# Kernel tuning notes

Measured on AMD Instinct MI355X. Metric: run time of the kernel, lower is better.

Reference implementation:

```python
import jax, jax.numpy as jnp
import numpy as np
import math

B, S, IN_DIM = 4, 2048, 512
D, H, L, FF = 256, 4, 4, 2048
HD = D // H
EPS = 1e-5


def _pos_encoding(S, D, dtype=jnp.float32):
    pos = jnp.arange(S, dtype=jnp.float32)[:, None]
    div = jnp.exp(jnp.arange(0, D, 2, dtype=jnp.float32) * (-math.log(10000.0) / D))
    pe = jnp.zeros((S, D), dtype=jnp.float32)
    pe = pe.at[:, 0::2].set(jnp.sin(pos * div))
    pe = pe.at[:, 1::2].set(jnp.cos(pos * div))
    return pe.astype(dtype)


def _layernorm(x, w, b):
    mu = jnp.mean(x, axis=-1, keepdims=True)
    var = jnp.var(x, axis=-1, keepdims=True)
    return (x - mu) * jax.lax.rsqrt(var + EPS) * w + b


def setup_inputs() -> dict:
    key = jax.random.key(0)
    ks = jax.random.split(key, 12)
    sc = 0.02
    inp = {
        "x": jax.random.normal(ks[0], (B, S, IN_DIM), dtype=jnp.float32),
        "W_in": jax.random.normal(ks[1], (D, IN_DIM), dtype=jnp.float32) * sc,
        "b_in": jnp.zeros((D,), dtype=jnp.float32),
        "qkv_w": jax.random.normal(ks[2], (L, 3 * D, D), dtype=jnp.float32) * sc,
        "qkv_b": jnp.zeros((L, 3 * D), dtype=jnp.float32),
        "out_w": jax.random.normal(ks[3], (L, D, D), dtype=jnp.float32) * sc,
        "out_b": jnp.zeros((L, D), dtype=jnp.float32),
        "ln1_w": jnp.ones((L, D), dtype=jnp.float32),
        "ln1_b": jnp.zeros((L, D), dtype=jnp.float32),
        "ff1_w": jax.random.normal(ks[4], (L, FF, D), dtype=jnp.float32) * sc,
        "ff1_b": jnp.zeros((L, FF), dtype=jnp.float32),
        "ff2_w": jax.random.normal(ks[5], (L, D, FF), dtype=jnp.float32) * sc,
        "ff2_b": jnp.zeros((L, D), dtype=jnp.float32),
        "ln2_w": jnp.ones((L, D), dtype=jnp.float32),
        "ln2_b": jnp.zeros((L, D), dtype=jnp.float32),
        "W_fc": jax.random.normal(ks[6], (IN_DIM, D), dtype=jnp.float32) * sc,
        "b_fc": jnp.zeros((IN_DIM,), dtype=jnp.float32),
    }
    return inp


def reference(x, W_in, b_in, qkv_w, qkv_b, out_w, out_b, ln1_w, ln1_b,
              ff1_w, ff1_b, ff2_w, ff2_b, ln2_w, ln2_b, W_fc, b_fc):
    # input projection + positional encoding (dropout=0 / eval)
    h = jnp.einsum('bsi,di->bsd', x, W_in) + b_in
    h = h + _pos_encoding(S, D, h.dtype)[None]

    scale = 1.0 / math.sqrt(HD)
    for l in range(L):
        # --- self-attention (unfused: explicit QK^T + softmax + V) ---
        qkv = jnp.einsum('bsd,ed->bse', h, qkv_w[l]) + qkv_b[l]  # [B,S,3D]
        q, k, v = jnp.split(qkv, 3, axis=-1)
        q = q.reshape(B, S, H, HD).transpose(0, 2, 1, 3)  # [B,H,S,HD]
        k = k.reshape(B, S, H, HD).transpose(0, 2, 1, 3)
        v = v.reshape(B, S, H, HD).transpose(0, 2, 1, 3)
        scores = jnp.einsum('bhqd,bhkd->bhqk', q, k) * scale  # [B,H,S,S]
        attn = jax.nn.softmax(scores, axis=-1)
        ctx = jnp.einsum('bhqk,bhkd->bhqd', attn, v)
        ctx = ctx.transpose(0, 2, 1, 3).reshape(B, S, D)
        sa = jnp.einsum('bsd,ed->bse', ctx, out_w[l]) + out_b[l]
        h = _layernorm(h + sa, ln1_w[l], ln1_b[l])  # post-norm
        # --- feed-forward (relu) ---
        ff = jax.nn.relu(jnp.einsum('bsd,fd->bsf', h, ff1_w[l]) + ff1_b[l])
        ff = jnp.einsum('bsf,df->bsd', ff, ff2_w[l]) + ff2_b[l]
        h = _layernorm(h + ff, ln2_w[l], ln2_b[l])

    # final projection from last time step
    return jnp.einsum('bd,od->bo', h[:, -1, :], W_fc) + b_fc  # [B, IN_DIM]
```

## Files before the change

kernel.cpp:

```cpp
#include <hip/hip_runtime.h>
#include <math.h>

#define S_LEN 2048
#define DMODEL 256
#define NHEAD 4
#define HDIM 64
#define NLAYER 4
#define FFDIM 2048
#define INDIM 512
#define BATCH 4
#define NTOK (BATCH * S_LEN)
#define EPSV 1e-5f
#define KSPLIT 4

typedef __attribute__((ext_vector_type(8))) short frag8;
typedef __attribute__((ext_vector_type(4))) float f32x4v;
typedef unsigned short u16;
typedef unsigned int u32;

__device__ __forceinline__ float pe_val(int s, int d) {
    const float c = 0.035977892f;
    float dv = expf(-(float)(d & ~1) * c);
    float arg = (float)s * dv;
    return (d & 1) ? cosf(arg) : sinf(arg);
}

__device__ __forceinline__ u16 f2bf(float f) {
    union { float f; unsigned u; } v; v.f = f;
    unsigned r = v.u + 0x7fffu + ((v.u >> 16) & 1u);
    return (u16)(r >> 16);
}
__device__ __forceinline__ float bf2f(u16 h) {
    union { u32 u; float f; } v; v.u = (u32)h << 16; return v.f;
}
__device__ __forceinline__ u32 pk2bf(float lo, float hi) {
    union { float f; u32 u; } a, b; a.f = lo; b.f = hi;
    return __builtin_amdgcn_perm(b.u, a.u, 0x07060302u);
}
__device__ __forceinline__ void load_lds16(const u16* g, u16* l) {
    __builtin_amdgcn_global_load_lds(
        (const __attribute__((address_space(1))) unsigned int*)g,
        (__attribute__((address_space(3))) unsigned int*)l, 16, 0, 0);
}

__global__ __launch_bounds__(256) void cvt_all(
    const float* __restrict__ x, const float* __restrict__ W_in,
    const float* __restrict__ qkv_w, const float* __restrict__ out_w,
    const float* __restrict__ ff1_w, const float* __restrict__ ff2_w,
    u16* __restrict__ xb, u16* __restrict__ W_in_b,
    u16* __restrict__ qkv_w_b, u16* __restrict__ out_w_b,
    u16* __restrict__ ff1_w_b, u16* __restrict__ ff2_w_b)
{
    const int i = blockIdx.x * 256 + threadIdx.x;
    const float* src; u16* dst; int base;
    if (i < 1048576)      { src = x;     dst = xb;      base = 0; }
    else if (i < 1081344) { src = W_in;  dst = W_in_b;  base = 1048576; }
    else if (i < 1277952) { src = qkv_w; dst = qkv_w_b; base = 1081344; }
    else if (i < 1343488) { src = out_w; dst = out_w_b; base = 1277952; }
    else if (i < 1867776) { src = ff1_w; dst = ff1_w_b; base = 1343488; }
    else                  { src = ff2_w; dst = ff2_w_b; base = 1867776; }
    const int e = (i - base) * 4;
    const float4 v = *(const float4*)(src + e);
    ushort4 o;
    o.x = f2bf(v.x); o.y = f2bf(v.y); o.z = f2bf(v.z); o.w = f2bf(v.w);
    *(ushort4*)(dst + e) = o;
}

template <int MODE>
__global__ __launch_bounds__(256) void gemm_mfma(
    const u16* __restrict__ A, const u16* __restrict__ W,
    const float* __restrict__ bias, u16* __restrict__ Cb,
    u16* __restrict__ vt, int M, int N, int K)
{
    __shared__ __align__(16) u16 As[128 * 32];
    __shared__ __align__(16) u16 Bs[128 * 32];
    const int t = threadIdx.x;
    const int w = t >> 6, lane = t & 63;
    const int col = lane & 15, quad = lane >> 4;
    const int qx = (quad ^ ((col >> 1) & 3)) * 8;
    const int m0 = blockIdx.x * 128, n0 = blockIdx.y * 128;
    const int wm = (w >> 1) * 64, wn = (w & 1) * 64;

    const int r0 = lane >> 2;
    const int kc = ((lane & 3) ^ ((lane >> 3) & 3)) * 8;
    const u16* pA0 = A + (size_t)(m0 + (w * 2 + 0) * 16 + r0) * K + kc;
    const u16* pA1 = A + (size_t)(m0 + (w * 2 + 1) * 16 + r0) * K + kc;
    const u16* pB0 = W + (size_t)(n0 + (w * 2 + 0) * 16 + r0) * K + kc;
    const u16* pB1 = W + (size_t)(n0 + (w * 2 + 1) * 16 + r0) * K + kc;
    u16* lA0 = As + (w * 2 + 0) * 512;
    u16* lA1 = As + (w * 2 + 1) * 512;
    u16* lB0 = Bs + (w * 2 + 0) * 512;
    u16* lB1 = Bs + (w * 2 + 1) * 512;

    f32x4v acc[4][4];
#pragma unroll
    for (int i = 0; i < 4; ++i)
#pragma unroll
        for (int j = 0; j < 4; ++j) acc[i][j] = (f32x4v){0.f, 0.f, 0.f, 0.f};

    for (int kb = 0; kb < K; kb += 32) {
        __syncthreads();
        load_lds16(pA0 + kb, lA0);
        load_lds16(pA1 + kb, lA1);
        load_lds16(pB0 + kb, lB0);
        load_lds16(pB1 + kb, lB1);
        __syncthreads();

        frag8 a[4], b[4];
#pragma unroll
        for (int i = 0; i < 4; ++i)
            a[i] = *(const frag8*)&As[(wm + i * 16 + col) * 32 + qx];
#pragma unroll
        for (int j = 0; j < 4; ++j)
            b[j] = *(const frag8*)&Bs[(wn + j * 16 + col) * 32 + qx];
#pragma unroll
        for (int i = 0; i < 4; ++i)
#pragma unroll
            for (int j = 0; j < 4; ++j)
                acc[i][j] = __builtin_amdgcn_mfma_f32_16x16x32_bf16(
                    a[i], b[j], acc[i][j], 0, 0, 0);
    }

#pragma unroll
    for (int j = 0; j < 4; ++j) {
        const int cn = n0 + wn + j * 16 + col;
        const float bv = bias[cn];
#pragma unroll
        for (int i = 0; i < 4; ++i) {
            const int cmb = m0 + wm + i * 16 + quad * 4;
            float vv[4];
#pragma unroll
            for (int r = 0; r < 4; ++r) {
                float v = acc[i][j][r] + bv;
                if (MODE == 2) v = fmaxf(v, 0.f);
                vv[r] = v;
                Cb[(size_t)(cmb + r) * N + cn] = f2bf(v);
            }
            if (MODE == 4 && cn >= 512) {
                const int dg = cn - 512;
                const int bh = (cmb >> 11) * 4 + (dg >> 6);
                uint2 pk;
                pk.x = ((u32)f2bf(vv[1]) << 16) | f2bf(vv[0]);
                pk.y = ((u32)f2bf(vv[3]) << 16) | f2bf(vv[2]);
                *(uint2*)&vt[((size_t)bh * 64 + (dg & 63)) * S_LEN + (cmb & 2047)] = pk;
            }
        }
    }
}

template <int MODE>
__global__ __launch_bounds__(256) void gemm64k(
    const u16* __restrict__ A, const u16* __restrict__ W,
    const float* __restrict__ bias, u16* __restrict__ Cb,
    int M, int N, int K)
{
    __shared__ __align__(16) u16 As[64 * 64];
    __shared__ __align__(16) u16 Bs[64 * 64];
    const int t = threadIdx.x;
    const int w = t >> 6, lane = t & 63;
    const int col = lane & 15, quad = lane >> 4;
    const int px0 = ((quad ^ (col & 7))) * 8;
    const int px1 = px0 ^ 32;
    const int m0 = blockIdx.x * 64, n0 = blockIdx.y * 64;
    const int wm = (w >> 1) * 32, wn = (w & 1) * 32;

    const int sr = lane >> 3;
    const int lc = ((lane & 7) ^ sr) * 8;
    const u16* pA0 = A + (size_t)(m0 + w * 16 + sr) * K + lc;
    const u16* pA1 = A + (size_t)(m0 + w * 16 + 8 + sr) * K + lc;
    const u16* pB0 = W + (size_t)(n0 + w * 16 + sr) * K + lc;
    const u16* pB1 = W + (size_t)(n0 + w * 16 + 8 + sr) * K + lc;
    u16* lA0 = As + (w * 16) * 64;
    u16* lA1 = As + (w * 16 + 8) * 64;
    u16* lB0 = Bs + (w * 16) * 64;
    u16* lB1 = Bs + (w * 16 + 8) * 64;

    f32x4v acc[2][2];
#pragma unroll
    for (int i = 0; i < 2; ++i)
#pragma unroll
        for (int j = 0; j < 2; ++j) acc[i][j] = (f32x4v){0.f, 0.f, 0.f, 0.f};

    for (int kb = 0; kb < K; kb += 64) {
        __syncthreads();
        load_lds16(pA0 + kb, lA0);
        load_lds16(pA1 + kb, lA1);
        load_lds16(pB0 + kb, lB0);
        load_lds16(pB1 + kb, lB1);
        __syncthreads();

#pragma unroll
        for (int kh = 0; kh < 2; ++kh) {
            const int px = kh ? px1 : px0;
            frag8 a[2], b[2];
#pragma unroll
            for (int i = 0; i < 2; ++i)
                a[i] = *(const frag8*)&As[(wm + i * 16 + col) * 64 + px];
#pragma unroll
            for (int j = 0; j < 2; ++j)
                b[j] = *(const frag8*)&Bs[(wn + j * 16 + col) * 64 + px];
#pragma unroll
            for (int i = 0; i < 2; ++i)
#pragma unroll
                for (int j = 0; j < 2; ++j)
                    acc[i][j] = __builtin_amdgcn_mfma_f32_16x16x32_bf16(
                        a[i], b[j], acc[i][j], 0, 0, 0);
        }
    }

#pragma unroll
    for (int j = 0; j < 2; ++j) {
        const int cn = n0 + wn + j * 16 + col;
        const float bv = bias[cn];
#pragma unroll
        for (int i = 0; i < 2; ++i) {
#pragma unroll
            for (int r = 0; r < 4; ++r) {
                const int cm = m0 + wm + i * 16 + quad * 4 + r;
                float v = acc[i][j][r] + bv;
                if (MODE == 1) v += pe_val(cm & (S_LEN - 1), cn);
                Cb[(size_t)cm * N + cn] = f2bf(v);
            }
        }
    }
}

__global__ __launch_bounds__(256) void attn_part(const u16* __restrict__ qkv,
                                                 const u16* __restrict__ vt,
                                                 float* __restrict__ Opart,
                                                 float* __restrict__ lpart)
{
    __shared__ __align__(16) u16 Ks0[64 * 32], Ks1[64 * 32];
    __shared__ __align__(16) u16 Vt0[64 * 32], Vt1[64 * 32];
    __shared__ __align__(16) u16 Ps[4][2][2][512];

    const int t = threadIdx.x;
    const int w = t >> 6, lane = t & 63;
    const int col = lane & 15, quad = lane >> 4;
    const int sq = (col >> 1) & 3;
    const int qx = (quad ^ sq) * 8;
    const int bh = blockIdx.x, b = bh >> 2, hh = bh & 3;
    const int qt = blockIdx.y, ks = blockIdx.z;

    const float SCL = 0.125f * 1.44269504f;

    frag8 qf[2][2];
#pragma unroll
    for (int qg = 0; qg < 2; ++qg) {
        const int qrow = qt * 128 + w * 32 + qg * 16 + col;
        const u16* qp = qkv + (size_t)(b * S_LEN + qrow) * 768 + hh * HDIM;
        const frag8 r0 = *(const frag8*)(qp + quad * 8);
        const frag8 r1 = *(const frag8*)(qp + 32 + quad * 8);
#pragma unroll
        for (int e = 0; e < 8; ++e) {
            qf[qg][0][e] = (short)f2bf(bf2f((u16)r0[e]) * SCL);
            qf[qg][1][e] = (short)f2bf(bf2f((u16)r1[e]) * SCL);
        }
    }

    f32x4v Oacc[2][4];
#pragma unroll
    for (int qg = 0; qg < 2; ++qg)
#pragma unroll
        for (int dt = 0; dt < 4; ++dt) Oacc[qg][dt] = (f32x4v){0.f, 0.f, 0.f, 0.f};
    float lsum[2] = {0.f, 0.f};

    const int srow = w * 16 + (lane >> 2);
    const int sseg = ((lane & 3) ^ ((lane >> 3) & 3)) * 8;
    const int kb0 = ks * (S_LEN / KSPLIT);
    const u16* kbase = qkv + (size_t)(b * S_LEN + kb0 + srow) * 768
                       + 256 + hh * HDIM + sseg;
    const u16* vbase = vt + ((size_t)bh * 64 + srow) * S_LEN + kb0 + sseg;
    u16* lK0 = Ks0 + w * 512;
    u16* lK1 = Ks1 + w * 512;
    u16* lV0 = Vt0 + w * 512;
    u16* lV1 = Vt1 + w * 512;

    for (int kt = 0; kt < S_LEN / KSPLIT / 64; ++kt) {
        __syncthreads();
        const u16* kp = kbase + (size_t)kt * 64 * 768;
        const u16* vp = vbase + kt * 64;
        load_lds16(kp, lK0);
        load_lds16(kp + 32, lK1);
        load_lds16(vp, lV0);
        load_lds16(vp + 32, lV1);
        __syncthreads();

#pragma unroll
        for (int nt = 0; nt < 4; ++nt) {
            const frag8 k0 = *(const frag8*)&Ks0[(nt * 16 + col) * 32 + qx];
            const frag8 k1 = *(const frag8*)&Ks1[(nt * 16 + col) * 32 + qx];
            const int c = (nt & 1) * 2 + (quad >> 1);
            const int poff = col * 32 + ((c ^ sq) * 8) + (quad & 1) * 4;
#pragma unroll
            for (int qg = 0; qg < 2; ++qg) {
                f32x4v s = (f32x4v){0.f, 0.f, 0.f, 0.f};
                s = __builtin_amdgcn_mfma_f32_16x16x32_bf16(k0, qf[qg][0], s, 0, 0, 0);
                s = __builtin_amdgcn_mfma_f32_16x16x32_bf16(k1, qf[qg][1], s, 0, 0, 0);
                const float p0 = __builtin_amdgcn_exp2f(s[0]);
                const float p1 = __builtin_amdgcn_exp2f(s[1]);
                const float p2 = __builtin_amdgcn_exp2f(s[2]);
                const float p3 = __builtin_amdgcn_exp2f(s[3]);
                lsum[qg] += (p0 + p1) + (p2 + p3);
                uint2 pk;
                pk.x = pk2bf(p0, p1);
                pk.y = pk2bf(p2, p3);
                *(uint2*)&Ps[w][qg][nt >> 1][poff] = pk;
            }
        }

        frag8 pf[2][2];
#pragma unroll
        for (int qg = 0; qg < 2; ++qg) {
            pf[qg][0] = *(const frag8*)&Ps[w][qg][0][col * 32 + qx];
            pf[qg][1] = *(const frag8*)&Ps[w][qg][1][col * 32 + qx];
        }
#pragma unroll
        for (int dt = 0; dt < 4; ++dt) {
            const frag8 v0 = *(const frag8*)&Vt0[(dt * 16 + col) * 32 + qx];
            const frag8 v1 = *(const frag8*)&Vt1[(dt * 16 + col) * 32 + qx];
#pragma unroll
            for (int qg = 0; qg < 2; ++qg) {
                Oacc[qg][dt] = __builtin_amdgcn_mfma_f32_16x16x32_bf16(
                    v0, pf[qg][0], Oacc[qg][dt], 0, 0, 0);
                Oacc[qg][dt] = __builtin_amdgcn_mfma_f32_16x16x32_bf16(
                    v1, pf[qg][1], Oacc[qg][dt], 0, 0, 0);
            }
        }
    }

#pragma unroll
    for (int qg = 0; qg < 2; ++qg) {
        float ls = lsum[qg];
        ls += __shfl_xor(ls, 16);
        ls += __shfl_xor(ls, 32);
        const int qrow = qt * 128 + w * 32 + qg * 16 + col;
        float* op = Opart + (((size_t)ks * 16 + bh) * S_LEN + qrow) * 64;
#pragma unroll
        for (int dt = 0; dt < 4; ++dt) {
            float4 o;
            o.x = Oacc[qg][dt][0]; o.y = Oacc[qg][dt][1];
            o.z = Oacc[qg][dt][2]; o.w = Oacc[qg][dt][3];
            *(float4*)(op + dt * 16 + quad * 4) = o;
        }
        if (quad == 0)
            lpart[((size_t)ks * 16 + bh) * S_LEN + qrow] = ls;
    }
}

__global__ __launch_bounds__(256) void attn_combine(const float* __restrict__ Opart,
                                                    const float* __restrict__ lpart,
                                                    u16* __restrict__ ctx)
{
    const int idx = blockIdx.x * 256 + threadIdx.x;
    const int d4 = idx & 15;
    const int q = (idx >> 4) & (S_LEN - 1);
    const int bh = idx >> 15;
    const int b = bh >> 2, hh = bh & 3;

    float4 o = {0.f, 0.f, 0.f, 0.f};
    float l = 0.f;
#pragma unroll
    for (int ks = 0; ks < KSPLIT; ++ks) {
        const float4 po = *(const float4*)&Opart[
            (((size_t)ks * 16 + bh) * S_LEN + q) * 64 + d4 * 4];
        o.x += po.x; o.y += po.y; o.z += po.z; o.w += po.w;
        l += lpart[((size_t)ks * 16 + bh) * S_LEN + q];
    }
    const float inv = 1.f / l;
    ushort4 r;
    r.x = f2bf(o.x * inv); r.y = f2bf(o.y * inv);
    r.z = f2bf(o.z * inv); r.w = f2bf(o.w * inv);
    *(ushort4*)&ctx[((size_t)(b * S_LEN + q)) * DMODEL + hh * HDIM + d4 * 4] = r;
}

__global__ __launch_bounds__(256) void add_ln(u16* __restrict__ hb,
                                              const u16* __restrict__ r,
                                              const float* __restrict__ w,
                                              const float* __restrict__ b)
{
    const int t = blockIdx.x;
    const int d = threadIdx.x;
    const size_t idx = (size_t)t * DMODEL + d;
    const float x = bf2f(hb[idx]) + bf2f(r[idx]);

    float s = x, s2 = x * x;
#pragma unroll
    for (int off = 32; off; off >>= 1) {
        s += __shfl_down(s, off);
        s2 += __shfl_down(s2, off);
    }
    __shared__ float ls[4], ls2[4];
    __shared__ float mu_s, rs_s;
    const int wid = d >> 6, lane = d & 63;
    if (lane == 0) { ls[wid] = s; ls2[wid] = s2; }
    __syncthreads();
    if (d == 0) {
        const float ts = ls[0] + ls[1] + ls[2] + ls[3];
        const float ts2 = ls2[0] + ls2[1] + ls2[2] + ls2[3];
        const float mu = ts * (1.f / DMODEL);
        const float var = ts2 * (1.f / DMODEL) - mu * mu;
        mu_s = mu;
        rs_s = rsqrtf(var + EPSV);
    }
    __syncthreads();
    hb[idx] = f2bf((x - mu_s) * rs_s * w[d] + b[d]);
}

__global__ __launch_bounds__(256) void final_proj(const u16* __restrict__ hb,
                                                  const float* __restrict__ Wfc,
                                                  const float* __restrict__ bfc,
                                                  float* __restrict__ out)
{
    const int idx = blockIdx.x * 256 + threadIdx.x;
    const int b = idx >> 9;
    const int o = idx & 511;
    const u16* hp = hb + (size_t)(b * S_LEN + S_LEN - 1) * DMODEL;
    const float* wp = Wfc + (size_t)o * DMODEL;
    float s = 0.f;
#pragma unroll 4
    for (int d = 0; d < DMODEL; ++d) s += bf2f(hp[d]) * wp[d];
    out[idx] = s + bfc[o];
}

extern "C" void kernel_launch(void* const* d_in, const int* in_sizes, int n_in,
                              void* d_out, int out_size, void* d_ws, size_t ws_size,
                              hipStream_t stream)
{
    const float* x     = (const float*)d_in[0];
    const float* W_in  = (const float*)d_in[1];
    const float* b_in  = (const float*)d_in[2];
    const float* qkv_w = (const float*)d_in[3];
    const float* qkv_b = (const float*)d_in[4];
    const float* out_w = (const float*)d_in[5];
    const float* out_b = (const float*)d_in[6];
    const float* ln1_w = (const float*)d_in[7];
    const float* ln1_b = (const float*)d_in[8];
    const float* ff1_w = (const float*)d_in[9];
    const float* ff1_b = (const float*)d_in[10];
    const float* ff2_w = (const float*)d_in[11];
    const float* ff2_b = (const float*)d_in[12];
    const float* ln2_w = (const float*)d_in[13];
    const float* ln2_b = (const float*)d_in[14];
    const float* W_fc  = (const float*)d_in[15];
    const float* b_fc  = (const float*)d_in[16];
    float* out = (float*)d_out;

    char* p = (char*)d_ws;
    u16* hb    = (u16*)p;  p += (size_t)NTOK * DMODEL * 2;
    u16* sab   = (u16*)p;  p += (size_t)NTOK * DMODEL * 2;
    u16* xb    = (u16*)p;  p += (size_t)NTOK * INDIM * 2;
    u16* qkvb  = (u16*)p;  p += (size_t)NTOK * 768 * 2;
    u16* ctxb  = (u16*)p;  p += (size_t)NTOK * DMODEL * 2;
    u16* ffb   = (u16*)p;  p += (size_t)NTOK * FFDIM * 2;
    u16* vtb   = (u16*)p;  p += (size_t)16 * 64 * S_LEN * 2;
    u16* W_in_b  = (u16*)p; p += (size_t)131072 * 2;
    u16* qkv_w_b = (u16*)p; p += (size_t)786432 * 2;
    u16* out_w_b = (u16*)p; p += (size_t)262144 * 2;
    u16* ff1_w_b = (u16*)p; p += (size_t)2097152 * 2;
    u16* ff2_w_b = (u16*)p; p += (size_t)2097152 * 2;
    if (ws_size < (size_t)82051072) return;

    float* Opart = (float*)ffb;
    float* lpart = (float*)sab;

    cvt_all<<<9344, 256, 0, stream>>>(x, W_in, qkv_w, out_w, ff1_w, ff2_w,
                                      xb, W_in_b, qkv_w_b, out_w_b, ff1_w_b, ff2_w_b);

    gemm64k<1><<<dim3(NTOK / 64, DMODEL / 64), 256, 0, stream>>>(
        xb, W_in_b, b_in, hb, NTOK, DMODEL, INDIM);

    for (int l = 0; l < NLAYER; ++l) {
        gemm_mfma<4><<<dim3(NTOK / 128, 768 / 128), 256, 0, stream>>>(
            hb, qkv_w_b + (size_t)l * 768 * DMODEL, qkv_b + l * 768,
            qkvb, vtb, NTOK, 768, DMODEL);
        attn_part<<<dim3(BATCH * NHEAD, S_LEN / 128, KSPLIT), 256, 0, stream>>>(
            qkvb, vtb, Opart, lpart);
        attn_combine<<<2048, 256, 0, stream>>>(Opart, lpart, ctxb);
        gemm64k<0><<<dim3(NTOK / 64, DMODEL / 64), 256, 0, stream>>>(
            ctxb, out_w_b + (size_t)l * DMODEL * DMODEL, out_b + l * DMODEL,
            sab, NTOK, DMODEL, DMODEL);
        add_ln<<<NTOK, 256, 0, stream>>>(hb, sab, ln1_w + l * DMODEL, ln1_b + l * DMODEL);
        gemm_mfma<2><<<dim3(NTOK / 128, FFDIM / 128), 256, 0, stream>>>(
            hb, ff1_w_b + (size_t)l * FFDIM * DMODEL, ff1_b + l * FFDIM,
            ffb, nullptr, NTOK, FFDIM, DMODEL);
        gemm64k<0><<<dim3(NTOK / 64, DMODEL / 64), 256, 0, stream>>>(
            ffb, ff2_w_b + (size_t)l * DMODEL * FFDIM, ff2_b + l * DMODEL,
            sab, NTOK, DMODEL, FFDIM);
        add_ln<<<NTOK, 256, 0, stream>>>(hb, sab, ln2_w + l * DMODEL, ln2_b + l * DMODEL);
    }

    final_proj<<<8, 256, 0, stream>>>(hb, W_fc, b_fc, out);
}
```

Measured before the change: 569.9 us.

## Fuse residual into GEMM epilogue, bf16 attention partials, MFMA row sums, 64-tile QKV

Several changes land together. The residual add moves into the output-projection and FF2 GEMM epilogues (mode 5), so the layernorm kernel only reads one tensor. Attention partial outputs are stored as bf16 instead of fp32, roughly halving the traffic of the split-K partials. Softmax row sums are now accumulated with an MFMA against a ones vector, replacing the scalar adds and shuffles. The QKV projection also moves from the 128-tile GEMM to the 64-tile GEMM to get more blocks. The trade-offs are precision loss from the bf16 partials and extra MFMA work.

Result: no change. 566.7 us (-0.6%).

```diff
diff --git a/kernel.cpp b/kernel.cpp
--- a/kernel.cpp
+++ b/kernel.cpp
@@ -70,7 +70,7 @@
 __global__ __launch_bounds__(256) void gemm_mfma(
     const u16* __restrict__ A, const u16* __restrict__ W,
     const float* __restrict__ bias, u16* __restrict__ Cb,
-    u16* __restrict__ vt, int M, int N, int K)
+    int M, int N, int K)
 {
     __shared__ __align__(16) u16 As[128 * 32];
     __shared__ __align__(16) u16 Bs[128 * 32];
@@ -128,21 +128,11 @@
 #pragma unroll
         for (int i = 0; i < 4; ++i) {
             const int cmb = m0 + wm + i * 16 + quad * 4;
-            float vv[4];
 #pragma unroll
             for (int r = 0; r < 4; ++r) {
                 float v = acc[i][j][r] + bv;
                 if (MODE == 2) v = fmaxf(v, 0.f);
-                vv[r] = v;
                 Cb[(size_t)(cmb + r) * N + cn] = f2bf(v);
-            }
-            if (MODE == 4 && cn >= 512) {
-                const int dg = cn - 512;
-                const int bh = (cmb >> 11) * 4 + (dg >> 6);
-                uint2 pk;
-                pk.x = ((u32)f2bf(vv[1]) << 16) | f2bf(vv[0]);
-                pk.y = ((u32)f2bf(vv[3]) << 16) | f2bf(vv[2]);
-                *(uint2*)&vt[((size_t)bh * 64 + (dg & 63)) * S_LEN + (cmb & 2047)] = pk;
             }
         }
     }
@@ -152,7 +142,7 @@
 __global__ __launch_bounds__(256) void gemm64k(
     const u16* __restrict__ A, const u16* __restrict__ W,
     const float* __restrict__ bias, u16* __restrict__ Cb,
-    int M, int N, int K)
+    u16* __restrict__ aux, int M, int N, int K)
 {
     __shared__ __align__(16) u16 As[64 * 64];
     __shared__ __align__(16) u16 Bs[64 * 64];
@@ -214,12 +204,23 @@
         const float bv = bias[cn];
 #pragma unroll
         for (int i = 0; i < 2; ++i) {
+            const int cmb = m0 + wm + i * 16 + quad * 4;
+            float vv[4];
 #pragma unroll
             for (int r = 0; r < 4; ++r) {
-                const int cm = m0 + wm + i * 16 + quad * 4 + r;
                 float v = acc[i][j][r] + bv;
-                if (MODE == 1) v += pe_val(cm & (S_LEN - 1), cn);
-                Cb[(size_t)cm * N + cn] = f2bf(v);
+                if (MODE == 1) v += pe_val((cmb + r) & (S_LEN - 1), cn);
+                if (MODE == 5) v += bf2f(aux[(size_t)(cmb + r) * N + cn]);
+                vv[r] = v;
+                Cb[(size_t)(cmb + r) * N + cn] = f2bf(v);
+            }
+            if (MODE == 4 && cn >= 512) {
+                const int dg = cn - 512;
+                const int bh = (cmb >> 11) * 4 + (dg >> 6);
+                uint2 pk;
+                pk.x = ((u32)f2bf(vv[1]) << 16) | f2bf(vv[0]);
+                pk.y = ((u32)f2bf(vv[3]) << 16) | f2bf(vv[2]);
+                *(uint2*)&aux[((size_t)bh * 64 + (dg & 63)) * S_LEN + (cmb & 2047)] = pk;
             }
         }
     }
@@ -227,7 +228,7 @@
 
 __global__ __launch_bounds__(256) void attn_part(const u16* __restrict__ qkv,
                                                  const u16* __restrict__ vt,
-                                                 float* __restrict__ Opart,
+                                                 u16* __restrict__ Opart,
                                                  float* __restrict__ lpart)
 {
     __shared__ __align__(16) u16 Ks0[64 * 32], Ks1[64 * 32];
@@ -257,13 +258,17 @@
             qf[qg][1][e] = (short)f2bf(bf2f((u16)r1[e]) * SCL);
         }
     }
-
-    f32x4v Oacc[2][4];
-#pragma unroll
-    for (int qg = 0; qg < 2; ++qg)
+    frag8 ones;
+#pragma unroll
+    for (int e = 0; e < 8; ++e) ones[e] = (short)0x3F80;
+
+    f32x4v Oacc[2][4], lacc[2];
+#pragma unroll
+    for (int qg = 0; qg < 2; ++qg) {
 #pragma unroll
         for (int dt = 0; dt < 4; ++dt) Oacc[qg][dt] = (f32x4v){0.f, 0.f, 0.f, 0.f};
-    float lsum[2] = {0.f, 0.f};
+        lacc[qg] = (f32x4v){0.f, 0.f, 0.f, 0.f};
+    }
 
     const int srow = w * 16 + (lane >> 2);
     const int sseg = ((lane & 3) ^ ((lane >> 3) & 3)) * 8;
@@ -301,7 +306,6 @@
                 const float p1 = __builtin_amdgcn_exp2f(s[1]);
                 const float p2 = __builtin_amdgcn_exp2f(s[2]);
                 const float p3 = __builtin_amdgcn_exp2f(s[3]);
-                lsum[qg] += (p0 + p1) + (p2 + p3);
                 uint2 pk;
                 pk.x = pk2bf(p0, p1);
                 pk.y = pk2bf(p2, p3);
@@ -327,28 +331,32 @@
                     v1, pf[qg][1], Oacc[qg][dt], 0, 0, 0);
             }
         }
+#pragma unroll
+        for (int qg = 0; qg < 2; ++qg) {
+            lacc[qg] = __builtin_amdgcn_mfma_f32_16x16x32_bf16(
+                ones, pf[qg][0], lacc[qg], 0, 0, 0);
+            lacc[qg] = __builtin_amdgcn_mfma_f32_16x16x32_bf16(
+                ones, pf[qg][1], lacc[qg], 0, 0, 0);
+        }
     }
 
 #pragma unroll
     for (int qg = 0; qg < 2; ++qg) {
-        float ls = lsum[qg];
-        ls += __shfl_xor(ls, 16);
-        ls += __shfl_xor(ls, 32);
         const int qrow = qt * 128 + w * 32 + qg * 16 + col;
-        float* op = Opart + (((size_t)ks * 16 + bh) * S_LEN + qrow) * 64;
+        u16* op = Opart + (((size_t)ks * 16 + bh) * S_LEN + qrow) * 64;
 #pragma unroll
         for (int dt = 0; dt < 4; ++dt) {
-            float4 o;
-            o.x = Oacc[qg][dt][0]; o.y = Oacc[qg][dt][1];
-            o.z = Oacc[qg][dt][2]; o.w = Oacc[qg][dt][3];
-            *(float4*)(op + dt * 16 + quad * 4) = o;
+            uint2 pk;
+            pk.x = pk2bf(Oacc[qg][dt][0], Oacc[qg][dt][1]);
+            pk.y = pk2bf(Oacc[qg][dt][2], Oacc[qg][dt][3]);
+            *(uint2*)(op + dt * 16 + quad * 4) = pk;
         }
         if (quad == 0)
-            lpart[((size_t)ks * 16 + bh) * S_LEN + qrow] = ls;
-    }
-}
-
-__global__ __launch_bounds__(256) void attn_combine(const float* __restrict__ Opart,
+            lpart[((size_t)ks * 16 + bh) * S_LEN + qrow] = lacc[qg][0];
+    }
+}
+
+__global__ __launch_bounds__(256) void attn_combine(const u16* __restrict__ Opart,
                                                     const float* __restrict__ lpart,
                                                     u16* __restrict__ ctx)
 {
@@ -358,31 +366,31 @@
     const int bh = idx >> 15;
     const int b = bh >> 2, hh = bh & 3;
 
-    float4 o = {0.f, 0.f, 0.f, 0.f};
-    float l = 0.f;
+    float o0 = 0.f, o1 = 0.f, o2 = 0.f, o3 = 0.f, l = 0.f;
 #pragma unroll
     for (int ks = 0; ks < KSPLIT; ++ks) {
-        const float4 po = *(const float4*)&Opart[
+        const ushort4 po = *(const ushort4*)&Opart[
             (((size_t)ks * 16 + bh) * S_LEN + q) * 64 + d4 * 4];
-        o.x += po.x; o.y += po.y; o.z += po.z; o.w += po.w;
+        o0 += bf2f(po.x); o1 += bf2f(po.y);
+        o2 += bf2f(po.z); o3 += bf2f(po.w);
         l += lpart[((size_t)ks * 16 + bh) * S_LEN + q];
     }
     const float inv = 1.f / l;
     ushort4 r;
-    r.x = f2bf(o.x * inv); r.y = f2bf(o.y * inv);
-    r.z = f2bf(o.z * inv); r.w = f2bf(o.w * inv);
+    r.x = f2bf(o0 * inv); r.y = f2bf(o1 * inv);
+    r.z = f2bf(o2 * inv); r.w = f2bf(o3 * inv);
     *(ushort4*)&ctx[((size_t)(b * S_LEN + q)) * DMODEL + hh * HDIM + d4 * 4] = r;
 }
 
-__global__ __launch_bounds__(256) void add_ln(u16* __restrict__ hb,
-                                              const u16* __restrict__ r,
-                                              const float* __restrict__ w,
-                                              const float* __restrict__ b)
+__global__ __launch_bounds__(256) void ln_only(u16* __restrict__ hb,
+                                               const u16* __restrict__ sab,
+                                               const float* __restrict__ w,
+                                               const float* __restrict__ b)
 {
     const int t = blockIdx.x;
     const int d = threadIdx.x;
     const size_t idx = (size_t)t * DMODEL + d;
-    const float x = bf2f(hb[idx]) + bf2f(r[idx]);
+    const float x = bf2f(sab[idx]);
 
     float s = x, s2 = x * x;
 #pragma unroll
@@ -461,33 +469,33 @@
     u16* ff2_w_b = (u16*)p; p += (size_t)2097152 * 2;
     if (ws_size < (size_t)82051072) return;
 
-    float* Opart = (float*)ffb;
+    u16* Opart = ffb;
     float* lpart = (float*)sab;
 
     cvt_all<<<9344, 256, 0, stream>>>(x, W_in, qkv_w, out_w, ff1_w, ff2_w,
                                       xb, W_in_b, qkv_w_b, out_w_b, ff1_w_b, ff2_w_b);
 
     gemm64k<1><<<dim3(NTOK / 64, DMODEL / 64), 256, 0, stream>>>(
-        xb, W_in_b, b_in, hb, NTOK, DMODEL, INDIM);
+        xb, W_in_b, b_in, hb, nullptr, NTOK, DMODEL, INDIM);
 
     for (int l = 0; l < NLAYER; ++l) {
-        gemm_mfma<4><<<dim3(NTOK / 128, 768 / 128), 256, 0, stream>>>(
+        gemm64k<4><<<dim3(NTOK / 64, 768 / 64), 256, 0, stream>>>(
             hb, qkv_w_b + (size_t)l * 768 * DMODEL, qkv_b + l * 768,
             qkvb, vtb, NTOK, 768, DMODEL);
         attn_part<<<dim3(BATCH * NHEAD, S_LEN / 128, KSPLIT), 256, 0, stream>>>(
             qkvb, vtb, Opart, lpart);
         attn_combine<<<2048, 256, 0, stream>>>(Opart, lpart, ctxb);
-        gemm64k<0><<<dim3(NTOK / 64, DMODEL / 64), 256, 0, stream>>>(
+        gemm64k<5><<<dim3(NTOK / 64, DMODEL / 64), 256, 0, stream>>>(
             ctxb, out_w_b + (size_t)l * DMODEL * DMODEL, out_b + l * DMODEL,
-            sab, NTOK, DMODEL, DMODEL);
-        add_ln<<<NTOK, 256, 0, stream>>>(hb, sab, ln1_w + l * DMODEL, ln1_b + l * DMODEL);
+            sab, hb, NTOK, DMODEL, DMODEL);
+        ln_only<<<NTOK, 256, 0, stream>>>(hb, sab, ln1_w + l * DMODEL, ln1_b + l * DMODEL);
         gemm_mfma<2><<<dim3(NTOK / 128, FFDIM / 128), 256, 0, stream>>>(
             hb, ff1_w_b + (size_t)l * FFDIM * DMODEL, ff1_b + l * FFDIM,
-            ffb, nullptr, NTOK, FFDIM, DMODEL);
-        gemm64k<0><<<dim3(NTOK / 64, DMODEL / 64), 256, 0, stream>>>(
+            ffb, NTOK, FFDIM, DMODEL);
+        gemm64k<5><<<dim3(NTOK / 64, DMODEL / 64), 256, 0, stream>>>(
             ffb, ff2_w_b + (size_t)l * DMODEL * FFDIM, ff2_b + l * DMODEL,
-            sab, NTOK, DMODEL, FFDIM);
-        add_ln<<<NTOK, 256, 0, stream>>>(hb, sab, ln2_w + l * DMODEL, ln2_b + l * DMODEL);
+            sab, hb, NTOK, DMODEL, FFDIM);
+        ln_only<<<NTOK, 256, 0, stream>>>(hb, sab, ln2_w + l * DMODEL, ln2_b + l * DMODEL);
     }
 
     final_proj<<<8, 256, 0, stream>>>(hb, W_fc, b_fc, out);
```
